# Performance work log

Hardware: AMD Instinct MI355X
Metric: run time of the kernel (lower is better)

## Reference

```python
import jax, jax.numpy as jnp
import numpy as np

B, CTX, QST, E, H = 8, 4096, 512, 300, 128

def setup_inputs() -> dict:
    key = jax.random.key(0)
    k1, k2, k3, k4 = jax.random.split(key, 4)
    context_sequence = jax.random.normal(k1, (B, CTX, E), dtype=jnp.float32)
    question_sequence = jax.random.normal(k2, (B, QST, E), dtype=jnp.float32)
    question_mask = jnp.ones((B, QST), dtype=jnp.int32)
    # dense layer params (PyTorch Linear: y = x @ W.T + b)
    bound = 1.0 / np.sqrt(E)
    W = jax.random.uniform(k3, (H, E), minval=-bound, maxval=bound, dtype=jnp.float32)
    b = jax.random.uniform(k4, (H,), minval=-bound, maxval=bound, dtype=jnp.float32)
    return {"context_sequence": context_sequence, "question_sequence": question_sequence,
            "question_mask": question_mask, "W": W, "b": b}

def reference(context_sequence, question_sequence, question_mask, W, b):
    # ReLU(dense(x)) for both sequences
    ctx_logits = jax.nn.relu(jnp.einsum('bce,he->bch', context_sequence, W) + b)   # [B, CTX, H]
    qst_logits = jax.nn.relu(jnp.einsum('bqe,he->bqh', question_sequence, W) + b)  # [B, QST, H]
    scores = jnp.einsum('bch,bqh->bcq', ctx_logits, qst_logits)                    # [B, CTX, QST]
    scores = jnp.where(question_mask[:, None, :] == 0, -jnp.inf, scores)
    attn = jax.nn.softmax(scores, axis=-1)
    return jnp.einsum('bcq,bqh->bch', attn, qst_logits)                            # [B, CTX, H]
```

## Files before the change

kernel.cpp:

```cpp
#include <hip/hip_runtime.h>
#include <hip/hip_bf16.h>

#define BB   8
#define SCTX 4096
#define SQ   512
#define EE   300
#define HH   128
#define EP   320
#define CST  328
#define QCH  136
#define LOG2E 1.4426950408889634f

typedef short short8 __attribute__((ext_vector_type(8)));
typedef float f32x4  __attribute__((ext_vector_type(4)));

#define MFMA16(a, b, c) __builtin_amdgcn_mfma_f32_16x16x32_bf16((a), (b), (c), 0, 0, 0)

__device__ __forceinline__ short f2bf(float f) {
  unsigned u = __builtin_bit_cast(unsigned, f);
  u += 0x7fffu + ((u >> 16) & 1u);
  return (short)(u >> 16);
}

__global__ void k_wpad(const float* __restrict__ W, short* __restrict__ wsw) {
  const int h = blockIdx.x, k = threadIdx.x;
  float v = (k < EE) ? W[h * EE + k] : 0.0f;
  const int m = h >> 4, t = h & 15, kk = k >> 5, quad = (k >> 3) & 3, j = k & 7;
  wsw[((kk * 8 + m) * 64 + quad * 16 + t) * 8 + j] = f2bf(v);
}

__global__ __launch_bounds__(256) void k_qlog(const float* __restrict__ qst,
                                              const short* __restrict__ wsw,
                                              const float* __restrict__ bias,
                                              short* __restrict__ ql,
                                              short* __restrict__ qlT) {
  const int b = blockIdx.y;
  const int m0 = blockIdx.x * 32;
  const int tid = threadIdx.x;
  const int w = tid >> 6, l = tid & 63, t = l & 15, quad = l >> 4;
  const int g = w >> 1, hf = w & 1;

  __shared__ __align__(16) short cst[32 * CST];

  const float4* cbase = (const float4*)(qst + (size_t)(b * SQ + m0) * EE);
#pragma unroll
  for (int j = 0; j < 10; ++j) {
    int i4 = tid + j * 256;
    if (i4 < 2400) {
      float4 v = cbase[i4];
      int row = i4 / 75, c4 = i4 - row * 75;
      short* dp = cst + row * CST + c4 * 4;
      dp[0] = f2bf(v.x); dp[1] = f2bf(v.y); dp[2] = f2bf(v.z); dp[3] = f2bf(v.w);
    }
  }
  for (int i = tid; i < 320; i += 256) {
    int row = i / 10, c = (i - row * 10) * 2;
    cst[row * CST + 300 + c] = 0;
    cst[row * CST + 301 + c] = 0;
  }
  __syncthreads();

  const short* arow = cst + (g * 16 + t) * CST;
  f32x4 acc[4] = {};
#pragma unroll
  for (int kk = 0; kk < 10; ++kk) {
    const int k = kk * 32 + quad * 8;
    short8 a = *(const short8*)(arow + k);
#pragma unroll
    for (int n = 0; n < 4; ++n) {
      short8 w8 = *(const short8*)(wsw + ((kk * 8 + hf * 4 + n) * 64 + l) * 8);
      acc[n] = MFMA16(a, w8, acc[n]);
    }
  }
#pragma unroll
  for (int n = 0; n < 4; ++n) {
    const int h = (hf * 4 + n) * 16 + t;
    const float bv = bias[h];
#pragma unroll
    for (int r = 0; r < 4; ++r) {
      float v = fmaxf(acc[n][r] + bv, 0.0f);
      short s16 = f2bf(v);
      const int row = m0 + g * 16 + quad * 4 + r;
      ql[((size_t)b * SQ + row) * HH + h] = s16;
      qlT[((size_t)b * HH + h) * SQ + row] = s16;
    }
  }
}

__global__ __launch_bounds__(256, 2) void k_attn(const float* __restrict__ ctx,
                                                 const short* __restrict__ wsw,
                                                 const float* __restrict__ bias,
                                                 const int* __restrict__ mask,
                                                 const short* __restrict__ ql,
                                                 const short* __restrict__ qlT,
                                                 float* __restrict__ out) {
  const int b = blockIdx.y;
  const int m0 = blockIdx.x * 64;
  const int tid = threadIdx.x;
  const int w = tid >> 6, l = tid & 63, t = l & 15, quad = l >> 4;
  const int g = w >> 1, hf = w & 1;

  __shared__ __align__(16) short uq[17408];
  __shared__ __align__(16) short uc[8704];
  __shared__ float maskb[SQ];
  short* cst = uq;
  short* qch = uq;
  short* clt = uc;
  short* pbw = uc + w * 2176;

  for (int i = tid; i < SQ; i += 256)
    maskb[i] = mask[b * SQ + i] ? -8.0f : -1e30f;

  for (int i = 0; i < 2; ++i) {
    const float4* cbase = (const float4*)(ctx + ((size_t)b * SCTX + m0 + i * 32) * EE);
#pragma unroll
    for (int j = 0; j < 10; ++j) {
      int i4 = tid + j * 256;
      if (i4 < 2400) {
        float4 v = cbase[i4];
        int row = i4 / 75, c4 = i4 - row * 75;
        short* dp = cst + row * CST + c4 * 4;
        dp[0] = f2bf(v.x); dp[1] = f2bf(v.y); dp[2] = f2bf(v.z); dp[3] = f2bf(v.w);
      }
    }
    for (int k = tid; k < 320; k += 256) {
      int row = k / 10, c = (k - row * 10) * 2;
      cst[row * CST + 300 + c] = 0;
      cst[row * CST + 301 + c] = 0;
    }
    __syncthreads();
    const short* arow = cst + (g * 16 + t) * CST;
    f32x4 acc[4] = {};
#pragma unroll
    for (int kk = 0; kk < 10; ++kk) {
      const int k = kk * 32 + quad * 8;
      short8 a = *(const short8*)(arow + k);
#pragma unroll
      for (int n = 0; n < 4; ++n) {
        short8 w8 = *(const short8*)(wsw + ((kk * 8 + hf * 4 + n) * 64 + l) * 8);
        acc[n] = MFMA16(a, w8, acc[n]);
      }
    }
#pragma unroll
    for (int n = 0; n < 4; ++n) {
      const int h = (hf * 4 + n) * 16 + t;
      const float bv = bias[h];
#pragma unroll
      for (int r = 0; r < 4; ++r) {
        float v = fmaxf(acc[n][r] + bv, 0.0f);
        clt[(i * 32 + g * 16 + quad * 4 + r) * 136 + h] = f2bf(v);
      }
    }
    __syncthreads();
  }

  short8 af[4];
#pragma unroll
  for (int kk = 0; kk < 4; ++kk)
    af[kk] = *(const short8*)&clt[(w * 16 + t) * 136 + kk * 32 + quad * 8];
  __syncthreads();

  const short8* qsrc = (const short8*)(ql + (size_t)b * SQ * HH);
  const short8* vsrc = (const short8*)(qlT + (size_t)b * HH * SQ);

  f32x4 o[8] = {};
  f32x4 rsum = {0.f, 0.f, 0.f, 0.f};
  for (int c = 0; c < 4; ++c) {
#pragma unroll
    for (int j = 0; j < 8; ++j) {
      int i = tid + j * 256;
      *(short8*)&qch[(i >> 4) * QCH + (i & 15) * 8] = qsrc[c * 2048 + i];
    }
    __syncthreads();
#pragma unroll
    for (int n2 = 0; n2 < 8; ++n2) {
      f32x4 sv = {0.f, 0.f, 0.f, 0.f};
      const short* qrow = qch + (n2 * 16 + t) * QCH;
#pragma unroll
      for (int kk = 0; kk < 4; ++kk) {
        short8 b8 = *(const short8*)(qrow + kk * 32 + quad * 8);
        sv = MFMA16(af[kk], b8, sv);
      }
      const float mb = maskb[c * 128 + n2 * 16 + t];
#pragma unroll
      for (int r = 0; r < 4; ++r) {
        float p = exp2f((sv[r] + mb) * LOG2E);
        rsum[r] += p;
        pbw[(quad * 4 + r) * 136 + n2 * 16 + t] = f2bf(p);
      }
    }
    __syncthreads();
#pragma unroll
    for (int j = 0; j < 8; ++j) {
      int i = tid + j * 256;
      *(short8*)&qch[(i >> 4) * QCH + (i & 15) * 8] = vsrc[(i >> 4) * 64 + c * 16 + (i & 15)];
    }
    __syncthreads();
#pragma unroll
    for (int kk = 0; kk < 4; ++kk) {
      short8 pa = *(const short8*)&pbw[t * 136 + kk * 32 + quad * 8];
#pragma unroll
      for (int n = 0; n < 8; ++n) {
        short8 v8 = *(const short8*)&qch[(n * 16 + t) * QCH + kk * 32 + quad * 8];
        o[n] = MFMA16(pa, v8, o[n]);
      }
    }
    __syncthreads();
  }
#pragma unroll
  for (int off = 8; off; off >>= 1)
#pragma unroll
    for (int r = 0; r < 4; ++r) rsum[r] += __shfl_xor(rsum[r], off);

  f32x4 rinv;
#pragma unroll
  for (int r = 0; r < 4; ++r) rinv[r] = 1.0f / rsum[r];
  float* obase = out + ((size_t)b * SCTX + m0 + w * 16) * HH;
#pragma unroll
  for (int n = 0; n < 8; ++n)
#pragma unroll
    for (int r = 0; r < 4; ++r)
      obase[(quad * 4 + r) * HH + n * 16 + t] = o[n][r] * rinv[r];
}

extern "C" void kernel_launch(void* const* d_in, const int* in_sizes, int n_in,
                              void* d_out, int out_size, void* d_ws, size_t ws_size,
                              hipStream_t stream) {
  const float* ctx  = (const float*)d_in[0];
  const float* qst  = (const float*)d_in[1];
  const int*   mask = (const int*)d_in[2];
  const float* W    = (const float*)d_in[3];
  const float* bias = (const float*)d_in[4];
  float* out = (float*)d_out;

  short* wsw  = (short*)d_ws;
  short* ql   = (short*)((char*)d_ws + 81920);
  short* qlT  = ql + (size_t)BB * SQ * HH;

  k_wpad<<<dim3(HH), dim3(EP), 0, stream>>>(W, wsw);
  k_qlog<<<dim3(SQ / 32, BB), dim3(256), 0, stream>>>(qst, wsw, bias, ql, qlT);
  k_attn<<<dim3(SCTX / 64, BB), dim3(256), 0, stream>>>(ctx, wsw, bias, mask, ql, qlT, out);
}
```

Baseline: 122.8 us.

## Load Q and V MFMA operands directly from global instead of LDS staging

The attention phase no longer stages question-logit chunks (ql and qlT) through shared memory. Each wave now reads its MFMA B operands straight from global memory, relying on L1/L2 caching. This removes the cooperative LDS copies and four block-wide barriers per chunk, and shrinks the shared allocation, which may raise occupancy. The cost is that the four waves each fetch the same operands redundantly from cache with strided 16-byte accesses. The pbw buffer is per-wave, so dropping the barriers around it stays safe.

```diff
diff --git a/kernel.cpp b/kernel.cpp
--- a/kernel.cpp
+++ b/kernel.cpp
@@ -8,7 +8,6 @@
 #define HH   128
 #define EP   320
 #define CST  328
-#define QCH  136
 #define LOG2E 1.4426950408889634f
 
 typedef short short8 __attribute__((ext_vector_type(8)));
@@ -100,11 +99,9 @@
   const int w = tid >> 6, l = tid & 63, t = l & 15, quad = l >> 4;
   const int g = w >> 1, hf = w & 1;
 
-  __shared__ __align__(16) short uq[17408];
+  __shared__ __align__(16) short cst[32 * CST];
   __shared__ __align__(16) short uc[8704];
   __shared__ float maskb[SQ];
-  short* cst = uq;
-  short* qch = uq;
   short* clt = uc;
   short* pbw = uc + w * 2176;
 
@@ -160,27 +157,20 @@
     af[kk] = *(const short8*)&clt[(w * 16 + t) * 136 + kk * 32 + quad * 8];
   __syncthreads();
 
-  const short8* qsrc = (const short8*)(ql + (size_t)b * SQ * HH);
-  const short8* vsrc = (const short8*)(qlT + (size_t)b * HH * SQ);
+  const short8* qbase = (const short8*)ql + ((size_t)b * SQ + t) * 16 + quad;
+  const short8* vbase = (const short8*)qlT + ((size_t)b * HH + t) * 64 + quad;
 
   f32x4 o[8] = {};
   f32x4 rsum = {0.f, 0.f, 0.f, 0.f};
   for (int c = 0; c < 4; ++c) {
-#pragma unroll
-    for (int j = 0; j < 8; ++j) {
-      int i = tid + j * 256;
-      *(short8*)&qch[(i >> 4) * QCH + (i & 15) * 8] = qsrc[c * 2048 + i];
-    }
-    __syncthreads();
+    const short8* qc = qbase + c * 2048;
+    const short8* vc = vbase + c * 16;
 #pragma unroll
     for (int n2 = 0; n2 < 8; ++n2) {
       f32x4 sv = {0.f, 0.f, 0.f, 0.f};
-      const short* qrow = qch + (n2 * 16 + t) * QCH;
-#pragma unroll
-      for (int kk = 0; kk < 4; ++kk) {
-        short8 b8 = *(const short8*)(qrow + kk * 32 + quad * 8);
-        sv = MFMA16(af[kk], b8, sv);
-      }
+#pragma unroll
+      for (int kk = 0; kk < 4; ++kk)
+        sv = MFMA16(af[kk], qc[n2 * 256 + kk * 4], sv);
       const float mb = maskb[c * 128 + n2 * 16 + t];
 #pragma unroll
       for (int r = 0; r < 4; ++r) {
@@ -189,23 +179,13 @@
         pbw[(quad * 4 + r) * 136 + n2 * 16 + t] = f2bf(p);
       }
     }
-    __syncthreads();
-#pragma unroll
-    for (int j = 0; j < 8; ++j) {
-      int i = tid + j * 256;
-      *(short8*)&qch[(i >> 4) * QCH + (i & 15) * 8] = vsrc[(i >> 4) * 64 + c * 16 + (i & 15)];
-    }
-    __syncthreads();
 #pragma unroll
     for (int kk = 0; kk < 4; ++kk) {
       short8 pa = *(const short8*)&pbw[t * 136 + kk * 32 + quad * 8];
 #pragma unroll
-      for (int n = 0; n < 8; ++n) {
-        short8 v8 = *(const short8*)&qch[(n * 16 + t) * QCH + kk * 32 + quad * 8];
-        o[n] = MFMA16(pa, v8, o[n]);
-      }
-    }
-    __syncthreads();
+      for (int n = 0; n < 8; ++n)
+        o[n] = MFMA16(pa, vc[n * 1024 + kk * 4], o[n]);
+    }
   }
 #pragma unroll
   for (int off = 8; off; off >>= 1)
```

New measurement: 160.9 us. 1.31x slower.
